# Performance work log

Hardware: AMD Instinct MI355X
Metric: run time of the kernel (lower is better)

Reference implementation:

```python
import jax, jax.numpy as jnp
import numpy as np

B, CIN, N, E = 8192, 16, 96, 768
NF, EMB, NCLS = 64, 128, 210


def _p(key, shape, scale=0.05):
    return jax.random.normal(key, shape, dtype=jnp.float32) * scale


def setup_inputs() -> dict:
    key = jax.random.key(0)
    ks = jax.random.split(key, 20)
    return {
        "src": jax.random.normal(ks[0], (B, CIN, N), dtype=jnp.float32),
        "edge_index": jax.random.randint(ks[1], (2, E), 0, N, dtype=jnp.int32),
        "gcn1_w": _p(ks[2], (CIN, 64)), "gcn1_b": _p(ks[3], (64,)),
        "gcn2_w": _p(ks[4], (64, 32)), "gcn2_b": _p(ks[5], (32,)),
        "conv1_w": _p(ks[6], (NF, 32, 7)), "conv1_b": _p(ks[7], (NF,)),
        "conv2_w": _p(ks[8], (NF * 2, NF, 5)), "conv2_b": _p(ks[9], (NF * 2,)),
        "conv3_w": _p(ks[10], (NF * 4, NF * 2, 3)), "conv3_b": _p(ks[11], (NF * 4,)),
        "fc1_w": _p(ks[12], (3072, EMB)), "fc1_b": _p(ks[13], (EMB,)),
        "cls1_w": _p(ks[14], (EMB, EMB)), "cls1_b": _p(ks[15], (EMB,)),
        "cls2_w": _p(ks[16], (EMB, NCLS)), "cls2_b": _p(ks[17], (NCLS,)),
    }


def gcn_conv(x, edge_index, W, b):
    n = x.shape[1]
    loops = jnp.arange(n, dtype=edge_index.dtype)
    row = jnp.concatenate([edge_index[0], loops])  # targets
    col = jnp.concatenate([edge_index[1], loops])  # sources
    deg = jnp.zeros((n,), x.dtype).at[row].add(1.0)
    dinv = jax.lax.rsqrt(jnp.maximum(deg, 1e-12))
    norm = dinv[row] * dinv[col]                 # [E+N]
    h = x @ W                                    # [B, N, Fout]
    msgs = h[:, col, :] * norm[None, :, None]    # gather along node dim
    out = jnp.zeros_like(h).at[:, row, :].add(msgs)  # scatter-add
    return out + b


def conv1d(x, w, b, stride, pad):
    # x: [B, C, L], w: [O, C, K]
    y = jax.lax.conv_general_dilated(x, w, (stride,), [(pad, pad)],
                                     dimension_numbers=("NCH", "OIH", "NCH"))
    return y + b[None, :, None]


def reference(src, edge_index, gcn1_w, gcn1_b, gcn2_w, gcn2_b,
              conv1_w, conv1_b, conv2_w, conv2_b, conv3_w, conv3_b,
              fc1_w, fc1_b, cls1_w, cls1_b, cls2_w, cls2_b):
    x = jnp.transpose(src, (0, 2, 1))            # [B, N, CIN]
    x = jax.nn.relu(gcn_conv(x, edge_index, gcn1_w, gcn1_b))
    x = jax.nn.relu(gcn_conv(x, edge_index, gcn2_w, gcn2_b))
    x = jnp.transpose(x, (0, 2, 1))              # [B, 32, N]
    x = jax.nn.relu(conv1d(x, conv1_w, conv1_b, 2, 3))
    x = jax.nn.relu(conv1d(x, conv2_w, conv2_b, 2, 2))
    x = jax.nn.relu(conv1d(x, conv3_w, conv3_b, 2, 1))
    x = x.reshape(x.shape[0], -1)                # [B, 3072]
    feat = x @ fc1_w + fc1_b
    x = jax.nn.relu(feat)
    x = jax.nn.relu(x @ cls1_w + cls1_b)
    x = x @ cls2_w + cls2_b
    return (x, feat)
```

## Files before the change

kernel.cpp:

```cpp
#include <hip/hip_runtime.h>


typedef __attribute__((ext_vector_type(8))) short short8v;
typedef __attribute__((ext_vector_type(4))) float floatx4;

#define N_NODE 96
#define E_TOT  864
#define BATCH  8192ull

#define R0_OFF   0ull
#define R1_OFF   25165824ull
#define FR_OFF   50331648ull
#define R2_OFF   51380224ull
#define WT_OFF   52428800ull
#define W1N_OFF  (WT_OFF + 0)
#define W2N_OFF  (WT_OFF + 2048)
#define WC1_OFF  (WT_OFF + 4096)
#define WC2_OFF  (WT_OFF + 18432)
#define WC3_OFF  (WT_OFF + 59392)
#define WF1_OFF  (WT_OFF + 157696)
#define WL1_OFF  (WT_OFF + 550912)
#define WL2_OFF  (WT_OFF + 567296)
#define AH_OFF   (WT_OFF + 600064)

__device__ __forceinline__ unsigned short f2b(float f) {
    unsigned int u = __builtin_bit_cast(unsigned int, f);
    u += 0x7fffu + ((u >> 16) & 1u);
    return (unsigned short)(u >> 16);
}
__device__ __forceinline__ float b2f(unsigned short h) {
    unsigned int u = ((unsigned int)h) << 16;
    return __builtin_bit_cast(float, u);
}

__global__ void prep_all(const int* __restrict__ eidx,
                         const float* __restrict__ g1w, const float* __restrict__ g2w,
                         const float* __restrict__ w1, const float* __restrict__ w2,
                         const float* __restrict__ w3, const float* __restrict__ f1,
                         const float* __restrict__ l1, const float* __restrict__ l2,
                         unsigned short* __restrict__ wt,
                         unsigned short* __restrict__ adense) {
    __shared__ int rowv[E_TOT];
    __shared__ int colv[E_TOT];
    __shared__ int degi[N_NODE];
    __shared__ float dinv[N_NODE];
    __shared__ float ad[96 * 96];
    const int tid = threadIdx.x;
    if (blockIdx.x == 0) {
        for (int e = tid; e < E_TOT; e += 256) {
            int r, c;
            if (e < 768) { r = eidx[e]; c = eidx[768 + e]; }
            else         { r = e - 768; c = r; }
            rowv[e] = r; colv[e] = c;
        }
        for (int n = tid; n < N_NODE; n += 256) degi[n] = 0;
        for (int i = tid; i < 9216; i += 256) ad[i] = 0.f;
        __syncthreads();
        for (int e = tid; e < E_TOT; e += 256) atomicAdd(&degi[rowv[e]], 1);
        __syncthreads();
        for (int n = tid; n < N_NODE; n += 256)
            dinv[n] = rsqrtf(fmaxf((float)degi[n], 1e-12f));
        __syncthreads();
        for (int e = tid; e < E_TOT; e += 256)
            atomicAdd(&ad[rowv[e] * 96 + colv[e]], dinv[rowv[e]] * dinv[colv[e]]);
        __syncthreads();
        for (int i = tid; i < 9216; i += 256) adense[i] = f2b(ad[i]);
        return;
    }
    long idx = (long)(blockIdx.x - 1) * 256 + tid;
    if (idx >= 600064) return;
    float v;
    if (idx < 2048) {
        int o = idx >> 5, c = idx & 31;
        v = (c < 16) ? g1w[c * 64 + o] : 0.f;
    } else if (idx < 4096) {
        long j = idx - 2048; int g = j >> 6, c = j & 63;
        v = g2w[c * 32 + g];
    } else {
        long base, KS;
        int region;
        if      (idx < 18432)  { base = 4096;   KS = 7;  region = 0; }
        else if (idx < 59392)  { base = 18432;  KS = 10; region = 1; }
        else if (idx < 157696) { base = 59392;  KS = 12; region = 2; }
        else if (idx < 550912) { base = 157696; KS = 96; region = 3; }
        else if (idx < 567296) { base = 550912; KS = 4;  region = 4; }
        else                   { base = 567296; KS = 4;  region = 5; }
        long local = idx - base;
        long g  = local / (KS * 512);
        long rm = local % (KS * 512);
        long ks = rm / 512;
        int lane = (int)((rm % 512) / 8);
        int j    = (int)(rm % 8);
        int quad = lane >> 4, n16 = lane & 15;
        int n = (int)(g * 16 + n16);
        int k = (int)(ks * 32 + quad * 8 + j);
        switch (region) {
            case 0: { int t = k / 32,  c = k % 32;  v = w1[n * 224 + c * 7 + t]; } break;
            case 1: { int t = k / 64,  c = k % 64;  v = w2[n * 320 + c * 5 + t]; } break;
            case 2: { int t = k / 128, c = k % 128; v = w3[n * 384 + c * 3 + t]; } break;
            case 3: { int t = k / 256, o = k % 256; v = f1[(o * 12 + t) * 128 + n]; } break;
            case 4: v = l1[k * 128 + n]; break;
            default: v = (n < 210) ? l2[k * 210 + n] : 0.f; break;
        }
    }
    wt[idx] = f2b(v);
}

__launch_bounds__(256)
__global__ void gcn_fused(const float* __restrict__ src,
                          const unsigned short* __restrict__ adense,
                          const unsigned short* __restrict__ w1n,
                          const unsigned short* __restrict__ w2n,
                          const float* __restrict__ b1,
                          const float* __restrict__ b2,
                          unsigned short* __restrict__ h2) {
    __shared__ __align__(16) unsigned short pool[39936];
    float* FLT = (float*)pool;
    unsigned short* AH2  = pool;
    unsigned short* HW2T = pool;
    unsigned short* Xt   = pool + 13312;
    unsigned short* AH5  = pool + 13312;
    unsigned short* XA   = pool + 19968;
    unsigned short* H1S  = pool + 35328;

    const int tid = threadIdx.x;
    const int w = tid >> 6, lane = tid & 63, quad = lane >> 4, m16 = lane & 15;
    const size_t b0 = (size_t)blockIdx.x * 4;

    short8v w1f[4], w2f[2][2];
    float bv1[4], bv2[2];
#pragma unroll
    for (int fn = 0; fn < 4; fn++) {
        w1f[fn] = *(const short8v*)&w1n[(fn * 16 + m16) * 32 + quad * 8];
        bv1[fn] = b1[fn * 16 + m16];
    }
#pragma unroll
    for (int fn = 0; fn < 2; fn++) {
#pragma unroll
        for (int kk = 0; kk < 2; kk++)
            w2f[fn][kk] = *(const short8v*)&w2n[(fn * 16 + m16) * 64 + kk * 32 + quad * 8];
        bv2[fn] = b2[fn * 16 + m16];
    }

    for (int u = tid; u < 1536; u += 256) {
        int bl = u / 384, j = u % 384;
        *(float4*)&FLT[bl * 1544 + j * 4] = *(const float4*)&src[(b0 + bl) * 1536 + j * 4];
    }
    {
        short8v z = {0, 0, 0, 0, 0, 0, 0, 0};
        for (int u = tid; u < 768; u += 256)
            *(short8v*)&XA[(u >> 1) * 40 + 16 + (u & 1) * 8] = z;
    }
    __syncthreads();

    for (int u = tid; u < 768; u += 256) {
        int col = u / 12, seg = u % 12;
        int bl = col >> 4, c = col & 15;
        const float* f = &FLT[bl * 1544 + c * 96 + seg * 8];
        unsigned int d[4];
#pragma unroll
        for (int i = 0; i < 4; i++)
            d[i] = (unsigned int)f2b(f[2 * i]) | ((unsigned int)f2b(f[2 * i + 1]) << 16);
        *(uint4*)&Xt[col * 104 + seg * 8] = make_uint4(d[0], d[1], d[2], d[3]);
    }
    __syncthreads();

    for (int u = tid; u < 1152; u += 256) {
        int r = u / 12, q = u % 12;
        *(short8v*)&AH2[r * 104 + q * 8] = *(const short8v*)&adense[r * 96 + q * 8];
    }
    __syncthreads();

    {
        floatx4 acc[6] = {};
#pragma unroll
        for (int kk = 0; kk < 96; kk += 32) {
            short8v bfr = *(const short8v*)&Xt[(w * 16 + m16) * 104 + kk + quad * 8];
#pragma unroll
            for (int fm = 0; fm < 6; fm++) {
                short8v afr = *(const short8v*)&AH2[(fm * 16 + m16) * 104 + kk + quad * 8];
                acc[fm] = __builtin_amdgcn_mfma_f32_16x16x32_bf16(afr, bfr, acc[fm], 0, 0, 0);
            }
        }
#pragma unroll
        for (int fm = 0; fm < 6; fm++)
#pragma unroll
            for (int r = 0; r < 4; r++) {
                int node = fm * 16 + quad * 4 + r;
                XA[(node * 4 + w) * 40 + m16] = f2b(acc[fm][r]);
            }
    }
    __syncthreads();

    unsigned short* H1W = H1S + w * 1152;
    for (int cc = 0; cc < 6; cc++) {
        const int rowbase = w * 96 + cc * 16;
        short8v afr1 = *(const short8v*)&XA[(rowbase + m16) * 40 + quad * 8];
        floatx4 a1[4];
#pragma unroll
        for (int fn = 0; fn < 4; fn++) {
            floatx4 zc = {0.f, 0.f, 0.f, 0.f};
            a1[fn] = __builtin_amdgcn_mfma_f32_16x16x32_bf16(afr1, w1f[fn], zc, 0, 0, 0);
        }
#pragma unroll
        for (int fn = 0; fn < 4; fn++)
#pragma unroll
            for (int r = 0; r < 4; r++)
                H1W[(quad * 4 + r) * 72 + fn * 16 + m16] =
                    f2b(fmaxf(a1[fn][r] + bv1[fn], 0.f));
        floatx4 a2[2] = {};
#pragma unroll
        for (int kk = 0; kk < 2; kk++) {
            short8v afr2 = *(const short8v*)&H1W[m16 * 72 + kk * 32 + quad * 8];
#pragma unroll
            for (int fn = 0; fn < 2; fn++)
                a2[fn] = __builtin_amdgcn_mfma_f32_16x16x32_bf16(afr2, w2f[fn][kk], a2[fn], 0, 0, 0);
        }
#pragma unroll
        for (int fn = 0; fn < 2; fn++)
#pragma unroll
            for (int r = 0; r < 4; r++) {
                int row = rowbase + quad * 4 + r;
                int node = row >> 2, bl = row & 3;
                HW2T[(bl * 32 + fn * 16 + m16) * 104 + node] = f2b(a2[fn][r]);
            }
    }
    __syncthreads();

    for (int u = tid; u < 1152; u += 256) {
        int r = u / 12, q = u % 12;
        *(short8v*)&AH5[r * 104 + q * 8] = *(const short8v*)&adense[r * 96 + q * 8];
    }
    __syncthreads();

    {
        floatx4 acc[6][2] = {};
#pragma unroll
        for (int kk = 0; kk < 96; kk += 32) {
            short8v bfr[2];
#pragma unroll
            for (int fn = 0; fn < 2; fn++)
                bfr[fn] = *(const short8v*)&HW2T[(w * 32 + fn * 16 + m16) * 104 + kk + quad * 8];
#pragma unroll
            for (int fm = 0; fm < 6; fm++) {
                short8v afr = *(const short8v*)&AH5[(fm * 16 + m16) * 104 + kk + quad * 8];
#pragma unroll
                for (int fn = 0; fn < 2; fn++)
                    acc[fm][fn] = __builtin_amdgcn_mfma_f32_16x16x32_bf16(afr, bfr[fn], acc[fm][fn], 0, 0, 0);
            }
        }
#pragma unroll
        for (int fm = 0; fm < 6; fm++)
#pragma unroll
            for (int fn = 0; fn < 2; fn++)
#pragma unroll
                for (int r = 0; r < 4; r++) {
                    int node = fm * 16 + quad * 4 + r;
                    h2[((size_t)node * BATCH + b0 + w) * 32 + fn * 16 + m16] =
                        f2b(fmaxf(acc[fm][fn][r] + bv2[fn], 0.f));
                }
    }
}

template<int WM, int FN, int NTAP, int CIN, int NOUT, int STRIDE, int PAD, int LIN, int BK, int MODE>
__launch_bounds__(256)
__global__ void gemm_slab(const unsigned short* __restrict__ in,
                          const unsigned short* __restrict__ wn,
                          const float* __restrict__ bias,
                          unsigned short* __restrict__ outb,
                          float* __restrict__ outf) {
    constexpr int BM  = WM * 32;
    constexpr int BN  = FN * 32;
    constexpr int BKP = BK + 8;
    constexpr int CPT = CIN / BK;
    constexpr int NC  = NTAP * CPT;
    constexpr int KS  = NTAP * CIN / 32;
    constexpr int NV  = BM * BK / 8 / 256;
    constexpr int RPV = 256 / (BK / 8);
    constexpr int SZ1 = 2 * BM * BKP;
    constexpr int SZ2 = (MODE == 4) ? 16 : BM * (BN + 8);
    constexpr int POOL = SZ1 > SZ2 ? SZ1 : SZ2;
    __shared__ __align__(16) unsigned short pool[POOL];
    const int tid = threadIdx.x;
    const size_t b0 = blockIdx.x * BM;
    const int n0 = blockIdx.y * BN;
    const int l  = blockIdx.z;
    const int w = tid >> 6, lane = tid & 63, quad = lane >> 4, m16 = lane & 15;
    const int wm = w >> 1, wq = w & 1;
    const int mbase = wm * (WM * 16), nbase = wq * (FN * 16);
    const int gw = (n0 + nbase) >> 4;
    const int lr = tid / (BK / 8);
    const int lc = tid % (BK / 8);
    floatx4 acc[WM][FN] = {};
    const short8v zz8 = {0, 0, 0, 0, 0, 0, 0, 0};

    short8v pre[NV], nxt[NV];
    {
        int pos = STRIDE * l - PAD;
        if (pos >= 0 && pos < LIN) {
            const unsigned short* ag = in + ((size_t)pos * BATCH + b0) * CIN;
#pragma unroll
            for (int v = 0; v < NV; v++)
                pre[v] = *(const short8v*)&ag[(size_t)(lr + v * RPV) * CIN + lc * 8];
        } else {
#pragma unroll
            for (int v = 0; v < NV; v++) pre[v] = zz8;
        }
#pragma unroll
        for (int v = 0; v < NV; v++)
            *(short8v*)&pool[(lr + v * RPV) * BKP + lc * 8] = pre[v];
    }
    int p = 0;
#pragma unroll
    for (int ch = 0; ch < NC; ++ch) {
        __syncthreads();
        if (ch + 1 < NC) {
            int t = (ch + 1) / CPT, inner = (ch + 1) % CPT;
            int pos = STRIDE * l + t - PAD;
            if (pos >= 0 && pos < LIN) {
                const unsigned short* ag = in + ((size_t)pos * BATCH + b0) * CIN + inner * BK;
#pragma unroll
                for (int v = 0; v < NV; v++)
                    nxt[v] = *(const short8v*)&ag[(size_t)(lr + v * RPV) * CIN + lc * 8];
            } else {
#pragma unroll
                for (int v = 0; v < NV; v++) nxt[v] = zz8;
            }
        }
        const unsigned short* As = pool + p * BM * BKP;
        const int kbase = (ch / CPT) * CIN + (ch % CPT) * BK;
#pragma unroll
        for (int kk = 0; kk < BK; kk += 32) {
            const int ksG = (kbase + kk) >> 5;
            short8v bfr[FN];
#pragma unroll
            for (int fn = 0; fn < FN; fn++)
                bfr[fn] = *(const short8v*)&wn[(((size_t)(gw + fn) * KS + ksG) << 9) + lane * 8];
#pragma unroll
            for (int fm = 0; fm < WM; fm++) {
                short8v afr = *(const short8v*)&As[(mbase + fm * 16 + m16) * BKP + kk + quad * 8];
#pragma unroll
                for (int fn = 0; fn < FN; fn++)
                    acc[fm][fn] = __builtin_amdgcn_mfma_f32_16x16x32_bf16(afr, bfr[fn], acc[fm][fn], 0, 0, 0);
            }
        }
        if (ch + 1 < NC) {
            unsigned short* Ad = pool + (p ^ 1) * BM * BKP;
#pragma unroll
            for (int v = 0; v < NV; v++)
                *(short8v*)&Ad[(lr + v * RPV) * BKP + lc * 8] = nxt[v];
        }
        p ^= 1;
    }

    if constexpr (MODE == 4) {
#pragma unroll
        for (int fn = 0; fn < FN; fn++) {
            int cg = n0 + nbase + fn * 16 + m16;
            float bv = (cg < 210) ? bias[cg] : 0.f;
            if (cg < 210) {
#pragma unroll
                for (int fm = 0; fm < WM; fm++)
#pragma unroll
                    for (int r = 0; r < 4; r++) {
                        size_t row = b0 + mbase + fm * 16 + quad * 4 + r;
                        outf[row * 210 + cg] = acc[fm][fn][r] + bv;
                    }
            }
        }
    } else {
        float bv[FN];
#pragma unroll
        for (int fn = 0; fn < FN; fn++) bv[fn] = bias[n0 + nbase + fn * 16 + m16];
        __syncthreads();
        unsigned short* Cs = pool;
#pragma unroll
        for (int fm = 0; fm < WM; fm++)
#pragma unroll
            for (int r = 0; r < 4; r++) {
                int row = mbase + fm * 16 + quad * 4 + r;
#pragma unroll
                for (int fn = 0; fn < FN; fn++)
                    Cs[row * (BN + 8) + nbase + fn * 16 + m16] =
                        f2b(fmaxf(acc[fm][fn][r] + bv[fn], 0.f));
            }
        __syncthreads();
        for (int u = tid; u < BM * (BN / 8); u += 256) {
            int r = u / (BN / 8), cc = u % (BN / 8);
            *(short8v*)&outb[((size_t)l * BATCH + b0 + r) * NOUT + n0 + cc * 8] =
                *(short8v*)&Cs[r * (BN + 8) + cc * 8];
        }
    }
}

__launch_bounds__(256)
__global__ void fc1_splitk(const unsigned short* __restrict__ c3,
                           const unsigned short* __restrict__ wf1,
                           float* __restrict__ part) {
    __shared__ __align__(16) unsigned short pool[2 * 128 * 72];
    const int tid = threadIdx.x;
    const size_t b0 = blockIdx.x * 128;
    const int kg = blockIdx.z;
    const int w = tid >> 6, lane = tid & 63, quad = lane >> 4, m16 = lane & 15;
    const int wm = w >> 1, wq = w & 1;
    const int mbase = wm * 64, nbase = wq * 64;
    const int gw = nbase >> 4;
    const int lr = tid >> 3, lc = tid & 7;
    floatx4 acc[4][4] = {};
    short8v pre[4], nxt[4];

    {
        const unsigned short* ag = c3 + ((size_t)(kg * 2) * BATCH + b0) * 256;
#pragma unroll
        for (int v = 0; v < 4; v++)
            pre[v] = *(const short8v*)&ag[(size_t)(lr + v * 32) * 256 + lc * 8];
#pragma unroll
        for (int v = 0; v < 4; v++)
            *(short8v*)&pool[(lr + v * 32) * 72 + lc * 8] = pre[v];
    }
    int p = 0;
#pragma unroll
    for (int s = 0; s < 8; ++s) {
        __syncthreads();
        if (s + 1 < 8) {
            int t = kg * 2 + ((s + 1) >> 2), inner = (s + 1) & 3;
            const unsigned short* ag = c3 + ((size_t)t * BATCH + b0) * 256 + inner * 64;
#pragma unroll
            for (int v = 0; v < 4; v++)
                nxt[v] = *(const short8v*)&ag[(size_t)(lr + v * 32) * 256 + lc * 8];
        }
        const unsigned short* As = pool + p * 128 * 72;
        const int kbase = (kg * 2 + (s >> 2)) * 256 + (s & 3) * 64;
#pragma unroll
        for (int kk = 0; kk < 64; kk += 32) {
            const int ksG = (kbase + kk) >> 5;
            short8v bfr[4];
#pragma unroll
            for (int fn = 0; fn < 4; fn++)
                bfr[fn] = *(const short8v*)&wf1[(((size_t)(gw + fn) * 96 + ksG) << 9) + lane * 8];
#pragma unroll
            for (int fm = 0; fm < 4; fm++) {
                short8v afr = *(const short8v*)&As[(mbase + fm * 16 + m16) * 72 + kk + quad * 8];
#pragma unroll
                for (int fn = 0; fn < 4; fn++)
                    acc[fm][fn] = __builtin_amdgcn_mfma_f32_16x16x32_bf16(afr, bfr[fn], acc[fm][fn], 0, 0, 0);
            }
        }
        if (s + 1 < 8) {
            unsigned short* Ad = pool + (p ^ 1) * 128 * 72;
#pragma unroll
            for (int v = 0; v < 4; v++)
                *(short8v*)&Ad[(lr + v * 32) * 72 + lc * 8] = nxt[v];
        }
        p ^= 1;
    }
    float* pg = part + (size_t)kg * BATCH * 128;
#pragma unroll
    for (int fm = 0; fm < 4; fm++)
#pragma unroll
        for (int r = 0; r < 4; r++) {
            size_t row = b0 + mbase + fm * 16 + quad * 4 + r;
#pragma unroll
            for (int fn = 0; fn < 4; fn++)
                pg[row * 128 + nbase + fn * 16 + m16] = acc[fm][fn][r];
        }
}

__launch_bounds__(256)
__global__ void fc1_reduce(const float* __restrict__ part, const float* __restrict__ bias,
                           float* __restrict__ feat, unsigned short* __restrict__ fr) {
    const size_t idx = (size_t)blockIdx.x * 256 + threadIdx.x;
    const size_t row = idx >> 5;
    const int    c4  = (int)(idx & 31);
    float4 s = *(const float4*)&bias[c4 * 4];
#pragma unroll
    for (int z = 0; z < 6; z++) {
        float4 p = *(const float4*)&part[(z * BATCH + row) * 128 + c4 * 4];
        s.x += p.x; s.y += p.y; s.z += p.z; s.w += p.w;
    }
    *(float4*)&feat[row * 128 + c4 * 4] = s;
    unsigned int d0 = (unsigned int)f2b(fmaxf(s.x, 0.f)) |
                      ((unsigned int)f2b(fmaxf(s.y, 0.f)) << 16);
    unsigned int d1 = (unsigned int)f2b(fmaxf(s.z, 0.f)) |
                      ((unsigned int)f2b(fmaxf(s.w, 0.f)) << 16);
    *(uint2*)&fr[row * 128 + c4 * 4] = make_uint2(d0, d1);
}

extern "C" void kernel_launch(void* const* d_in, const int* in_sizes, int n_in,
                              void* d_out, int out_size, void* d_ws, size_t ws_size,
                              hipStream_t stream) {
    const float* src  = (const float*)d_in[0];
    const int*   eidx = (const int*)  d_in[1];
    const float* g1w  = (const float*)d_in[2];
    const float* g1b  = (const float*)d_in[3];
    const float* g2w  = (const float*)d_in[4];
    const float* g2b  = (const float*)d_in[5];
    const float* cv1w = (const float*)d_in[6];
    const float* cv1b = (const float*)d_in[7];
    const float* cv2w = (const float*)d_in[8];
    const float* cv2b = (const float*)d_in[9];
    const float* cv3w = (const float*)d_in[10];
    const float* cv3b = (const float*)d_in[11];
    const float* fc1w = (const float*)d_in[12];
    const float* fc1b = (const float*)d_in[13];
    const float* cl1w = (const float*)d_in[14];
    const float* cl1b = (const float*)d_in[15];
    const float* cl2w = (const float*)d_in[16];
    const float* cl2b = (const float*)d_in[17];

    unsigned short* ws16 = (unsigned short*)d_ws;
    float* wsF = (float*)d_ws;
    float* out = (float*)d_out;

    unsigned short* h2  = ws16 + R0_OFF;
    unsigned short* c1  = ws16 + R1_OFF;
    unsigned short* c2  = ws16 + R0_OFF;
    unsigned short* c3  = ws16 + R1_OFF;
    float*          part = wsF;
    unsigned short* fr  = ws16 + FR_OFF;
    unsigned short* r2  = ws16 + R2_OFF;
    unsigned short* w1n = ws16 + W1N_OFF;
    unsigned short* w2n = ws16 + W2N_OFF;
    unsigned short* wc1 = ws16 + WC1_OFF;
    unsigned short* wc2 = ws16 + WC2_OFF;
    unsigned short* wc3 = ws16 + WC3_OFF;
    unsigned short* wf1 = ws16 + WF1_OFF;
    unsigned short* wl1 = ws16 + WL1_OFF;
    unsigned short* wl2 = ws16 + WL2_OFF;
    unsigned short* ah  = ws16 + AH_OFF;

    float* feat_out = out + 8192ull * 210ull;

    prep_all<<<2346, 256, 0, stream>>>(eidx, g1w, g2w, cv1w, cv2w, cv3w, fc1w, cl1w, cl2w,
                                       ws16 + WT_OFF, ah);
    gcn_fused<<<2048, 256, 0, stream>>>(src, ah, w1n, w2n, g1b, g2b, h2);
    gemm_slab<8, 2, 7, 32, 64, 2, 3, 96, 32, 0>
        <<<dim3(32, 1, 48), 256, 0, stream>>>(h2, wc1, cv1b, c1, nullptr);
    gemm_slab<4, 4, 5, 64, 128, 2, 2, 48, 64, 0>
        <<<dim3(64, 1, 24), 256, 0, stream>>>(c1, wc2, cv2b, c2, nullptr);
    gemm_slab<4, 4, 3, 128, 256, 2, 1, 24, 64, 0>
        <<<dim3(64, 2, 12), 256, 0, stream>>>(c2, wc3, cv3b, c3, nullptr);
    fc1_splitk<<<dim3(64, 1, 6), 256, 0, stream>>>(c3, wf1, part);
    fc1_reduce<<<1024, 256, 0, stream>>>(part, fc1b, feat_out, fr);
    gemm_slab<2, 2, 1, 128, 128, 1, 0, 1, 64, 0>
        <<<dim3(128, 2, 1), 256, 0, stream>>>(fr, wl1, cl1b, r2, nullptr);
    gemm_slab<2, 2, 1, 128, 256, 1, 0, 1, 64, 4>
        <<<dim3(128, 4, 1), 256, 0, stream>>>(r2, wl2, cl2b, nullptr, out);
}
```

Measured before the change: 297.1 us.

## Restructure GCN kernel to per-wave private pipeline with pre-swizzled adjacency fragments

The adjacency matrix is now written by the prep kernel in MFMA fragment order, so each wave loads its A operands straight from global/L2 without staging through LDS. Each wave handles one sample independently: it loads src directly into B fragments with an in-register bf16 conversion, keeps intermediates in a small per-wave LDS region, and drops all block-wide __syncthreads. The output is staged in LDS and written with 16-byte coalesced stores. LDS use per block shrinks a lot, which lets launch bounds request higher occupancy. The cost is repeated global/L2 reads of the adjacency fragments by every wave.

```diff
diff --git a/kernel.cpp b/kernel.cpp
--- a/kernel.cpp
+++ b/kernel.cpp
@@ -39,7 +39,7 @@
                          const float* __restrict__ w3, const float* __restrict__ f1,
                          const float* __restrict__ l1, const float* __restrict__ l2,
                          unsigned short* __restrict__ wt,
-                         unsigned short* __restrict__ adense) {
+                         unsigned short* __restrict__ ahf) {
     __shared__ int rowv[E_TOT];
     __shared__ int colv[E_TOT];
     __shared__ int degi[N_NODE];
@@ -64,7 +64,14 @@
         for (int e = tid; e < E_TOT; e += 256)
             atomicAdd(&ad[rowv[e] * 96 + colv[e]], dinv[rowv[e]] * dinv[colv[e]]);
         __syncthreads();
-        for (int i = tid; i < 9216; i += 256) adense[i] = f2b(ad[i]);
+        for (int i = tid; i < 9216; i += 256) {
+            int f = i >> 9, rm = i & 511;
+            int ln = rm >> 3, j = rm & 7;
+            int fm = f / 3, kk = f % 3;
+            int row = fm * 16 + (ln & 15);
+            int col = kk * 32 + (ln >> 4) * 8 + j;
+            ahf[i] = f2b(ad[row * 96 + col]);
+        }
         return;
     }
     long idx = (long)(blockIdx.x - 1) * 256 + tid;
@@ -106,26 +113,23 @@
     wt[idx] = f2b(v);
 }
 
-__launch_bounds__(256)
+__launch_bounds__(256, 4)
 __global__ void gcn_fused(const float* __restrict__ src,
-                          const unsigned short* __restrict__ adense,
+                          const unsigned short* __restrict__ ahf,
                           const unsigned short* __restrict__ w1n,
                           const unsigned short* __restrict__ w2n,
                           const float* __restrict__ b1,
                           const float* __restrict__ b2,
                           unsigned short* __restrict__ h2) {
-    __shared__ __align__(16) unsigned short pool[39936];
-    float* FLT = (float*)pool;
-    unsigned short* AH2  = pool;
-    unsigned short* HW2T = pool;
-    unsigned short* Xt   = pool + 13312;
-    unsigned short* AH5  = pool + 13312;
-    unsigned short* XA   = pool + 19968;
-    unsigned short* H1S  = pool + 35328;
-
+    __shared__ __align__(16) unsigned short pool[4 * 4864];
     const int tid = threadIdx.x;
     const int w = tid >> 6, lane = tid & 63, quad = lane >> 4, m16 = lane & 15;
-    const size_t b0 = (size_t)blockIdx.x * 4;
+    unsigned short* P   = pool + w * 4864;
+    unsigned short* XAc = P;
+    unsigned short* H1W = P + 384;
+    unsigned short* HWT = P + 1536;
+    unsigned short* Cw  = P;
+    const size_t bb = (size_t)blockIdx.x * 4 + w;
 
     short8v w1f[4], w2f[2][2];
     float bv1[4], bv2[2];
@@ -142,60 +146,30 @@
         bv2[fn] = b2[fn * 16 + m16];
     }
 
-    for (int u = tid; u < 1536; u += 256) {
-        int bl = u / 384, j = u % 384;
-        *(float4*)&FLT[bl * 1544 + j * 4] = *(const float4*)&src[(b0 + bl) * 1536 + j * 4];
-    }
-    {
-        short8v z = {0, 0, 0, 0, 0, 0, 0, 0};
-        for (int u = tid; u < 768; u += 256)
-            *(short8v*)&XA[(u >> 1) * 40 + 16 + (u & 1) * 8] = z;
-    }
-    __syncthreads();
-
-    for (int u = tid; u < 768; u += 256) {
-        int col = u / 12, seg = u % 12;
-        int bl = col >> 4, c = col & 15;
-        const float* f = &FLT[bl * 1544 + c * 96 + seg * 8];
-        unsigned int d[4];
-#pragma unroll
-        for (int i = 0; i < 4; i++)
-            d[i] = (unsigned int)f2b(f[2 * i]) | ((unsigned int)f2b(f[2 * i + 1]) << 16);
-        *(uint4*)&Xt[col * 104 + seg * 8] = make_uint4(d[0], d[1], d[2], d[3]);
-    }
-    __syncthreads();
-
-    for (int u = tid; u < 1152; u += 256) {
-        int r = u / 12, q = u % 12;
-        *(short8v*)&AH2[r * 104 + q * 8] = *(const short8v*)&adense[r * 96 + q * 8];
-    }
-    __syncthreads();
-
-    {
-        floatx4 acc[6] = {};
-#pragma unroll
-        for (int kk = 0; kk < 96; kk += 32) {
-            short8v bfr = *(const short8v*)&Xt[(w * 16 + m16) * 104 + kk + quad * 8];
-#pragma unroll
-            for (int fm = 0; fm < 6; fm++) {
-                short8v afr = *(const short8v*)&AH2[(fm * 16 + m16) * 104 + kk + quad * 8];
-                acc[fm] = __builtin_amdgcn_mfma_f32_16x16x32_bf16(afr, bfr, acc[fm], 0, 0, 0);
-            }
-        }
-#pragma unroll
-        for (int fm = 0; fm < 6; fm++)
-#pragma unroll
-            for (int r = 0; r < 4; r++) {
-                int node = fm * 16 + quad * 4 + r;
-                XA[(node * 4 + w) * 40 + m16] = f2b(acc[fm][r]);
-            }
-    }
-    __syncthreads();
-
-    unsigned short* H1W = H1S + w * 1152;
+    floatx4 acc[6] = {};
+    const float* sB = src + bb * 1536 + (size_t)m16 * 96;
+#pragma unroll
+    for (int kk = 0; kk < 3; kk++) {
+        float4 f0 = *(const float4*)&sB[kk * 32 + quad * 8];
+        float4 f1 = *(const float4*)&sB[kk * 32 + quad * 8 + 4];
+        short8v bfr;
+        bfr[0] = (short)f2b(f0.x); bfr[1] = (short)f2b(f0.y);
+        bfr[2] = (short)f2b(f0.z); bfr[3] = (short)f2b(f0.w);
+        bfr[4] = (short)f2b(f1.x); bfr[5] = (short)f2b(f1.y);
+        bfr[6] = (short)f2b(f1.z); bfr[7] = (short)f2b(f1.w);
+#pragma unroll
+        for (int fm = 0; fm < 6; fm++) {
+            short8v afr = *(const short8v*)&ahf[((fm * 3 + kk) << 9) + lane * 8];
+            acc[fm] = __builtin_amdgcn_mfma_f32_16x16x32_bf16(afr, bfr, acc[fm], 0, 0, 0);
+        }
+    }
+
+#pragma unroll
     for (int cc = 0; cc < 6; cc++) {
-        const int rowbase = w * 96 + cc * 16;
-        short8v afr1 = *(const short8v*)&XA[(rowbase + m16) * 40 + quad * 8];
+#pragma unroll
+        for (int r = 0; r < 4; r++)
+            XAc[(quad * 4 + r) * 24 + m16] = f2b(acc[cc][r]);
+        short8v afr1 = *(const short8v*)&XAc[m16 * 24 + quad * 8];
         floatx4 a1[4];
 #pragma unroll
         for (int fn = 0; fn < 4; fn++) {
@@ -219,46 +193,39 @@
 #pragma unroll
         for (int fn = 0; fn < 2; fn++)
 #pragma unroll
-            for (int r = 0; r < 4; r++) {
-                int row = rowbase + quad * 4 + r;
-                int node = row >> 2, bl = row & 3;
-                HW2T[(bl * 32 + fn * 16 + m16) * 104 + node] = f2b(a2[fn][r]);
-            }
-    }
-    __syncthreads();
-
-    for (int u = tid; u < 1152; u += 256) {
-        int r = u / 12, q = u % 12;
-        *(short8v*)&AH5[r * 104 + q * 8] = *(const short8v*)&adense[r * 96 + q * 8];
-    }
-    __syncthreads();
-
-    {
-        floatx4 acc[6][2] = {};
-#pragma unroll
-        for (int kk = 0; kk < 96; kk += 32) {
-            short8v bfr[2];
+            for (int r = 0; r < 4; r++)
+                HWT[(fn * 16 + m16) * 104 + cc * 16 + quad * 4 + r] = f2b(a2[fn][r]);
+    }
+
+    floatx4 c2a[6][2] = {};
+#pragma unroll
+    for (int kk = 0; kk < 3; kk++) {
+        short8v bfr[2];
+#pragma unroll
+        for (int fn = 0; fn < 2; fn++)
+            bfr[fn] = *(const short8v*)&HWT[(fn * 16 + m16) * 104 + kk * 32 + quad * 8];
+#pragma unroll
+        for (int fm = 0; fm < 6; fm++) {
+            short8v afr = *(const short8v*)&ahf[((fm * 3 + kk) << 9) + lane * 8];
 #pragma unroll
             for (int fn = 0; fn < 2; fn++)
-                bfr[fn] = *(const short8v*)&HW2T[(w * 32 + fn * 16 + m16) * 104 + kk + quad * 8];
-#pragma unroll
-            for (int fm = 0; fm < 6; fm++) {
-                short8v afr = *(const short8v*)&AH5[(fm * 16 + m16) * 104 + kk + quad * 8];
-#pragma unroll
-                for (int fn = 0; fn < 2; fn++)
-                    acc[fm][fn] = __builtin_amdgcn_mfma_f32_16x16x32_bf16(afr, bfr[fn], acc[fm][fn], 0, 0, 0);
-            }
-        }
-#pragma unroll
-        for (int fm = 0; fm < 6; fm++)
-#pragma unroll
-            for (int fn = 0; fn < 2; fn++)
-#pragma unroll
-                for (int r = 0; r < 4; r++) {
-                    int node = fm * 16 + quad * 4 + r;
-                    h2[((size_t)node * BATCH + b0 + w) * 32 + fn * 16 + m16] =
-                        f2b(fmaxf(acc[fm][fn][r] + bv2[fn], 0.f));
-                }
+                c2a[fm][fn] = __builtin_amdgcn_mfma_f32_16x16x32_bf16(afr, bfr[fn], c2a[fm][fn], 0, 0, 0);
+        }
+    }
+#pragma unroll
+    for (int fm = 0; fm < 6; fm++)
+#pragma unroll
+        for (int fn = 0; fn < 2; fn++)
+#pragma unroll
+            for (int r = 0; r < 4; r++)
+                Cw[(fm * 16 + quad * 4 + r) * 32 + fn * 16 + m16] =
+                    f2b(fmaxf(c2a[fm][fn][r] + bv2[fn], 0.f));
+#pragma unroll
+    for (int it = 0; it < 6; it++) {
+        int idx = it * 64 + lane;
+        int node = idx >> 2, q8 = idx & 3;
+        *(uint4*)&h2[((size_t)node * BATCH + bb) * 32 + q8 * 8] =
+            *(const uint4*)&Cw[idx * 8];
     }
 }
 
@@ -527,13 +494,13 @@
     unsigned short* wf1 = ws16 + WF1_OFF;
     unsigned short* wl1 = ws16 + WL1_OFF;
     unsigned short* wl2 = ws16 + WL2_OFF;
-    unsigned short* ah  = ws16 + AH_OFF;
+    unsigned short* ahf = ws16 + AH_OFF;
 
     float* feat_out = out + 8192ull * 210ull;
 
     prep_all<<<2346, 256, 0, stream>>>(eidx, g1w, g2w, cv1w, cv2w, cv3w, fc1w, cl1w, cl2w,
-                                       ws16 + WT_OFF, ah);
-    gcn_fused<<<2048, 256, 0, stream>>>(src, ah, w1n, w2n, g1b, g2b, h2);
+                                       ws16 + WT_OFF, ahf);
+    gcn_fused<<<2048, 256, 0, stream>>>(src, ahf, w1n, w2n, g1b, g2b, h2);
     gemm_slab<8, 2, 7, 32, 64, 2, 3, 96, 32, 0>
         <<<dim3(32, 1, 48), 256, 0, stream>>>(h2, wc1, cv1b, c1, nullptr);
     gemm_slab<4, 4, 5, 64, 128, 2, 2, 48, 64, 0>
```

Result: faster. 274.5 us (-7.6%).
